# Optimization experiments

Hardware: AMD Instinct MI355X
Metric: run time of the kernel (lower is better)

## Reference

```python
import jax, jax.numpy as jnp
import numpy as np

N_NODES = 50000
N_EDGES = 300000
EMB = 256
HID = 512
L = 5
BN_EPS = 1e-5


def setup_inputs() -> dict:
    key = jax.random.key(0)
    ks = jax.random.split(key, 12)
    return {
        "node_ids": jax.random.randint(ks[0], (N_NODES,), 0, 100),
        "node_depth": jax.random.randint(ks[1], (N_NODES,), 0, 20),
        "edge_index": jax.random.randint(ks[2], (2, N_EDGES), 0, N_NODES),
        "edge_attr": jax.random.normal(ks[3], (N_EDGES, 2), jnp.float32),
        "node_type_emb": jax.random.normal(ks[4], (100, EMB), jnp.float32) * 0.1,
        "depth_emb": jax.random.normal(ks[5], (21, EMB), jnp.float32) * 0.1,
        "We": jax.random.normal(ks[6], (L, 2, EMB), jnp.float32) * 0.1,
        "be": jnp.zeros((L, EMB), jnp.float32),
        "W1": jax.random.normal(ks[7], (L, EMB, HID), jnp.float32) * (1.0 / np.sqrt(EMB)),
        "b1": jnp.zeros((L, HID), jnp.float32),
        "gamma": jnp.ones((L, HID), jnp.float32),
        "beta": jnp.zeros((L, HID), jnp.float32),
        "W2": jax.random.normal(ks[8], (L, HID, EMB), jnp.float32) * (1.0 / np.sqrt(HID)),
        "b2": jnp.zeros((L, EMB), jnp.float32),
        "eps_param": jnp.zeros((L,), jnp.float32),
    }


def reference(node_ids, node_depth, edge_index, edge_attr, node_type_emb,
              depth_emb, We, be, W1, b1, gamma, beta, W2, b2, eps_param):
    n = node_ids.shape[0]
    src, dst = edge_index[0], edge_index[1]
    # node encoder (code task): type embedding + clipped depth embedding
    depth = jnp.clip(node_depth, 0, depth_emb.shape[0] - 1)
    h = node_type_emb[node_ids] + depth_emb[depth]  # [N, EMB]
    n_layers = We.shape[0]
    for l in range(n_layers):
        e = edge_attr @ We[l] + be[l]  # [E, EMB] edge encoding
        msg = jax.nn.relu(h[src] + e)  # gather + relu
        agg = jax.ops.segment_sum(msg, dst, num_segments=n)  # scatter-add
        z = (1.0 + eps_param[l]) * h + agg
        # MLP: Linear -> BatchNorm1d (batch stats) -> ReLU -> Linear
        y = z @ W1[l] + b1[l]  # [N, HID]
        mu = jnp.mean(y, axis=0)
        var = jnp.var(y, axis=0)
        y = (y - mu) * jax.lax.rsqrt(var + BN_EPS) * gamma[l] + beta[l]
        y = jax.nn.relu(y)
        h_new = y @ W2[l] + b2[l]  # [N, EMB]
        if l < n_layers - 1:
            h_new = jax.nn.relu(h_new)  # dropout is identity (drop_ratio=0)
        h = h_new
    return h
```

## Files before the change

kernel.cpp:

```cpp
#include <hip/hip_runtime.h>

#define NN 50000
#define NE 300000
#define EMB 256
#define HID 512
#define NL 5

typedef __attribute__((ext_vector_type(8))) short bf16x8;
typedef __attribute__((ext_vector_type(4))) float f32x4;
typedef __attribute__((ext_vector_type(8))) unsigned short u16x8;
typedef __attribute__((ext_vector_type(4))) unsigned short u16x4;

union U8u { u16x8 v; unsigned short s[8]; };

__device__ __forceinline__ float bf2f(unsigned short u) {
  union { unsigned int i; float f; } c; c.i = ((unsigned int)u) << 16; return c.f;
}
__device__ __forceinline__ unsigned short f2bf(float f) {
  union { float f; unsigned int i; } c; c.f = f;
  unsigned int r = c.i + 0x7FFF + ((c.i >> 16) & 1);
  return (unsigned short)(r >> 16);
}

__global__ __launch_bounds__(256) void k_init_h(const int* __restrict__ ids,
    const int* __restrict__ depth, const float* __restrict__ temb,
    const float* __restrict__ demb, float* __restrict__ h) {
  int gid = blockIdx.x * 256 + threadIdx.x;
  int row = gid >> 6;
  if (row >= NN) return;
  int c4 = (gid & 63) << 2;
  int id = ids[row];
  int d = depth[row]; d = d < 0 ? 0 : (d > 20 ? 20 : d);
  float4 a = *(const float4*)&temb[id * EMB + c4];
  float4 b = *(const float4*)&demb[d * EMB + c4];
  *(float4*)&h[row * EMB + c4] = make_float4(a.x + b.x, a.y + b.y, a.z + b.z, a.w + b.w);
}

__global__ __launch_bounds__(256) void k_count(const int* __restrict__ dst, int* __restrict__ deg) {
  int e = blockIdx.x * 256 + threadIdx.x;
  if (e < NE) atomicAdd(&deg[dst[e]], 1);
}
__global__ __launch_bounds__(256) void k_scan1(const int* __restrict__ deg,
    int* __restrict__ row_off, int* __restrict__ bsums) {
  __shared__ int lds[256];
  int b = blockIdx.x, t = threadIdx.x;
  int base = b * 1024;
  int v[4]; int s = 0;
  for (int i = 0; i < 4; ++i) {
    int idx = base + t * 4 + i;
    v[i] = (idx < NN) ? deg[idx] : 0;
    s += v[i];
  }
  lds[t] = s; __syncthreads();
  for (int off = 1; off < 256; off <<= 1) {
    int x = (t >= off) ? lds[t - off] : 0; __syncthreads();
    lds[t] += x; __syncthreads();
  }
  int run = (t > 0) ? lds[t - 1] : 0;
  if (t == 255) bsums[b] = lds[255];
  for (int i = 0; i < 4; ++i) {
    int idx = base + t * 4 + i;
    if (idx < NN) row_off[idx] = run;
    run += v[i];
  }
}
__global__ __launch_bounds__(256) void k_scan2(int* __restrict__ bsums, int nb) {
  __shared__ int lds[256];
  int t = threadIdx.x;
  int v = (t < nb) ? bsums[t] : 0;
  lds[t] = v; __syncthreads();
  for (int off = 1; off < 256; off <<= 1) {
    int x = (t >= off) ? lds[t - off] : 0; __syncthreads();
    lds[t] += x; __syncthreads();
  }
  if (t < nb) bsums[t] = (t > 0) ? lds[t - 1] : 0;
}
__global__ __launch_bounds__(256) void k_scan3(int* __restrict__ row_off, const int* __restrict__ bsums) {
  int b = blockIdx.x, t = threadIdx.x;
  int base = b * 1024;
  int add = bsums[b];
  for (int i = 0; i < 4; ++i) {
    int idx = base + t * 4 + i;
    if (idx < NN) row_off[idx] += add;
  }
  if (b == 0 && t == 0) row_off[NN] = NE;
}
__global__ __launch_bounds__(256) void k_copy(const int* __restrict__ a, int* __restrict__ b) {
  int i = blockIdx.x * 256 + threadIdx.x;
  if (i < NN) b[i] = a[i];
}
__global__ __launch_bounds__(256) void k_fill(const int* __restrict__ src, const int* __restrict__ dst,
    const float* __restrict__ attr, int* __restrict__ cursor,
    int* __restrict__ ssrc, float2* __restrict__ sattr) {
  int e = blockIdx.x * 256 + threadIdx.x;
  if (e >= NE) return;
  int d = dst[e];
  int p = atomicAdd(&cursor[d], 1);
  ssrc[p] = src[e];
  sattr[p] = make_float2(attr[2 * e], attr[2 * e + 1]);
}

__global__ __launch_bounds__(256) void k_convW(const float* __restrict__ W,
    unsigned short* __restrict__ Wt, int R, int C) {
  __shared__ float t[32][33];
  int l = blockIdx.z;
  const float* Wl = W + (size_t)l * R * C;
  unsigned short* Wtl = Wt + (size_t)l * R * C;
  int c0 = blockIdx.x * 32, r0 = blockIdx.y * 32;
  int tx = threadIdx.x & 31, ty = threadIdx.x >> 5;
  for (int i = 0; i < 32; i += 8)
    t[ty + i][tx] = Wl[(size_t)(r0 + ty + i) * C + c0 + tx];
  __syncthreads();
  for (int i = 0; i < 32; i += 8)
    Wtl[(size_t)(c0 + ty + i) * R + r0 + tx] = f2bf(t[tx][ty + i]);
}

__global__ __launch_bounds__(256) void k_aggregate(const float* __restrict__ h,
    const int* __restrict__ row_off, const int* __restrict__ ssrc,
    const float2* __restrict__ sattr, const float* __restrict__ We_l,
    const float* __restrict__ be_l, const float* __restrict__ epsp, int layer,
    unsigned short* __restrict__ z) {
  int wid = (blockIdx.x * 256 + threadIdx.x) >> 6;
  if (wid >= NN) return;
  int c4 = (threadIdx.x & 63) << 2;
  float4 w0 = *(const float4*)&We_l[c4];
  float4 w1 = *(const float4*)&We_l[EMB + c4];
  float4 bb = *(const float4*)&be_l[c4];
  float4 acc = make_float4(0.f, 0.f, 0.f, 0.f);
  int k0 = row_off[wid], k1 = row_off[wid + 1];
  for (int k = k0; k < k1; ++k) {
    int s = ssrc[k];
    float2 a = sattr[k];
    float4 hv = *(const float4*)&h[(size_t)s * EMB + c4];
    acc.x += fmaxf(hv.x + a.x * w0.x + a.y * w1.x + bb.x, 0.f);
    acc.y += fmaxf(hv.y + a.x * w0.y + a.y * w1.y + bb.y, 0.f);
    acc.z += fmaxf(hv.z + a.x * w0.z + a.y * w1.z + bb.z, 0.f);
    acc.w += fmaxf(hv.w + a.x * w0.w + a.y * w1.w + bb.w, 0.f);
  }
  float e1 = 1.0f + epsp[layer];
  float4 hv = *(const float4*)&h[(size_t)wid * EMB + c4];
  u16x4 o;
  o[0] = f2bf(e1 * hv.x + acc.x);
  o[1] = f2bf(e1 * hv.y + acc.y);
  o[2] = f2bf(e1 * hv.z + acc.z);
  o[3] = f2bf(e1 * hv.w + acc.w);
  *(u16x4*)&z[(size_t)wid * EMB + c4] = o;
}

template<int K, int NC, int MODE>
__global__ __launch_bounds__(256) void k_mfma_gemm(
    const unsigned short* __restrict__ A, const unsigned short* __restrict__ Bt,
    const float* __restrict__ bias, const float* __restrict__ scale,
    const float* __restrict__ shift, unsigned short* __restrict__ Ybf,
    float* __restrict__ Hout, float* __restrict__ colsum, float* __restrict__ colsq) {
  __shared__ __align__(16) unsigned short lA[2][128 * 32];
  __shared__ __align__(16) unsigned short lB[2][128 * 32];
  int row0 = blockIdx.x * 128, col0 = blockIdx.y * 128;
  int tid = threadIdx.x, lane = tid & 63, wave = tid >> 6;
  int wr = (wave >> 1) * 64, wc = (wave & 1) * 64;
  int lr = lane & 15, lg = lane >> 4;
  f32x4 acc[4][4] = {};

  auto stageA = [&](int buf, int k0) {
#pragma unroll
    for (int r = 0; r < 2; ++r) {
      int off8 = (r * 256 + tid) * 8;
      int row = off8 >> 5;
      int kk = off8 & 31;
      int gr = row0 + row; if (gr > NN - 1) gr = NN - 1;
      u16x8 v = *(const u16x8*)&A[(size_t)gr * K + k0 + kk];
      if constexpr (MODE >= 1) {
        f32x4 sc0 = *(const f32x4*)&scale[k0 + kk];
        f32x4 sc1 = *(const f32x4*)&scale[k0 + kk + 4];
        f32x4 sh0 = *(const f32x4*)&shift[k0 + kk];
        f32x4 sh1 = *(const f32x4*)&shift[k0 + kk + 4];
        U8u u; u.v = v;
#pragma unroll
        for (int j = 0; j < 4; ++j)
          u.s[j] = f2bf(fmaxf(bf2f(u.s[j]) * sc0[j] + sh0[j], 0.f));
#pragma unroll
        for (int j = 0; j < 4; ++j)
          u.s[4 + j] = f2bf(fmaxf(bf2f(u.s[4 + j]) * sc1[j] + sh1[j], 0.f));
        v = u.v;
      }
      *(u16x8*)&lA[buf][off8] = v;
    }
  };
  auto stageB = [&](int buf, int k0) {
#pragma unroll
    for (int r = 0; r < 2; ++r) {
      int off8 = (r * 256 + tid) * 8;
      int col = off8 >> 5;
      int kk = off8 & 31;
      *(u16x8*)&lB[buf][off8] = *(const u16x8*)&Bt[(size_t)(col0 + col) * K + k0 + kk];
    }
  };

  int cur = 0;
  stageA(0, 0); stageB(0, 0);
  __syncthreads();
  for (int kt = 0; kt < K / 32; ++kt) {
    if (kt + 1 < K / 32) { stageA(cur ^ 1, (kt + 1) * 32); stageB(cur ^ 1, (kt + 1) * 32); }
    bf16x8 af[4], bfr[4];
#pragma unroll
    for (int m = 0; m < 4; ++m)
      af[m] = *(const bf16x8*)&lA[cur][(wr + m * 16 + lr) * 32 + lg * 8];
#pragma unroll
    for (int n = 0; n < 4; ++n)
      bfr[n] = *(const bf16x8*)&lB[cur][(wc + n * 16 + lr) * 32 + lg * 8];
#pragma unroll
    for (int m = 0; m < 4; ++m)
#pragma unroll
      for (int n = 0; n < 4; ++n)
        acc[m][n] = __builtin_amdgcn_mfma_f32_16x16x32_bf16(af[m], bfr[n], acc[m][n], 0, 0, 0);
    __syncthreads();
    cur ^= 1;
  }

  if constexpr (MODE == 0) {
    float cs[4] = {}, cq[4] = {};
#pragma unroll
    for (int n = 0; n < 4; ++n) {
      int gc = col0 + wc + n * 16 + lr;
      float bv = bias[gc];
#pragma unroll
      for (int m = 0; m < 4; ++m) {
        int grb = row0 + wr + m * 16 + lg * 4;
#pragma unroll
        for (int j = 0; j < 4; ++j) {
          int gr = grb + j;
          if (gr < NN) {
            float v = acc[m][n][j] + bv;
            Ybf[(size_t)gr * NC + gc] = f2bf(v);
            cs[n] += v; cq[n] += v * v;
          }
        }
      }
    }
#pragma unroll
    for (int n = 0; n < 4; ++n) {
      cs[n] += __shfl_xor(cs[n], 16, 64); cs[n] += __shfl_xor(cs[n], 32, 64);
      cq[n] += __shfl_xor(cq[n], 16, 64); cq[n] += __shfl_xor(cq[n], 32, 64);
    }
    if (lg == 0) {
#pragma unroll
      for (int n = 0; n < 4; ++n) {
        int gc = col0 + wc + n * 16 + lr;
        atomicAdd(&colsum[gc], cs[n]);
        atomicAdd(&colsq[gc], cq[n]);
      }
    }
  } else {
#pragma unroll
    for (int n = 0; n < 4; ++n) {
      int gc = col0 + wc + n * 16 + lr;
      float bv = bias[gc];
#pragma unroll
      for (int m = 0; m < 4; ++m) {
        int grb = row0 + wr + m * 16 + lg * 4;
#pragma unroll
        for (int j = 0; j < 4; ++j) {
          int gr = grb + j;
          if (gr < NN) {
            float v = acc[m][n][j] + bv;
            if constexpr (MODE == 1) v = fmaxf(v, 0.f);
            Hout[(size_t)gr * NC + gc] = v;
          }
        }
      }
    }
  }
}

__global__ void k_bnfin(const float* __restrict__ colsum, const float* __restrict__ colsq,
    const float* __restrict__ gamma, const float* __restrict__ beta,
    float* __restrict__ scale, float* __restrict__ shift) {
  int c = threadIdx.x;
  float inv_n = 1.0f / (float)NN;
  float mu = colsum[c] * inv_n;
  float var = colsq[c] * inv_n - mu * mu;
  float rstd = rsqrtf(var + 1e-5f);
  float sc = rstd * gamma[c];
  scale[c] = sc;
  shift[c] = beta[c] - mu * sc;
}

extern "C" void kernel_launch(void* const* d_in, const int* in_sizes, int n_in,
                              void* d_out, int out_size, void* d_ws, size_t ws_size,
                              hipStream_t stream) {
  (void)in_sizes; (void)n_in; (void)out_size; (void)ws_size;
  const int* node_ids    = (const int*)d_in[0];
  const int* node_depth  = (const int*)d_in[1];
  const int* edge_index  = (const int*)d_in[2];
  const float* edge_attr = (const float*)d_in[3];
  const float* temb      = (const float*)d_in[4];
  const float* demb      = (const float*)d_in[5];
  const float* We        = (const float*)d_in[6];
  const float* be        = (const float*)d_in[7];
  const float* W1        = (const float*)d_in[8];
  const float* b1        = (const float*)d_in[9];
  const float* gamma_    = (const float*)d_in[10];
  const float* beta_     = (const float*)d_in[11];
  const float* W2        = (const float*)d_in[12];
  const float* b2        = (const float*)d_in[13];
  const float* epsp      = (const float*)d_in[14];
  float* h = (float*)d_out;

  char* ws = (char*)d_ws;
  size_t off = 0;
  auto alloc = [&](size_t bytes) -> void* {
    void* p = ws + off;
    off = (off + bytes + 255) & ~(size_t)255;
    return p;
  };
  unsigned short* z   = (unsigned short*)alloc(2ull * NN * EMB);
  unsigned short* y   = (unsigned short*)alloc(2ull * NN * HID);
  unsigned short* W1t = (unsigned short*)alloc(2ull * NL * EMB * HID);
  unsigned short* W2t = (unsigned short*)alloc(2ull * NL * HID * EMB);
  int* deg      = (int*)alloc(sizeof(int) * NN);
  int* row_off  = (int*)alloc(sizeof(int) * (NN + 1));
  int* cursor   = (int*)alloc(sizeof(int) * NN);
  int* ssrc     = (int*)alloc(sizeof(int) * NE);
  float2* sattr = (float2*)alloc(sizeof(float2) * NE);
  int* bsums    = (int*)alloc(sizeof(int) * 256);
  float* colsum = (float*)alloc(sizeof(float) * HID * 2);
  float* colsq  = colsum + HID;
  float* scale  = (float*)alloc(sizeof(float) * HID);
  float* shift  = (float*)alloc(sizeof(float) * HID);

  const int* e_src = edge_index;
  const int* e_dst = edge_index + NE;

  k_init_h<<<(NN * 64) / 256, 256, 0, stream>>>(node_ids, node_depth, temb, demb, h);
  hipMemsetAsync(deg, 0, sizeof(int) * NN, stream);
  k_count<<<(NE + 255) / 256, 256, 0, stream>>>(e_dst, deg);
  k_scan1<<<49, 256, 0, stream>>>(deg, row_off, bsums);
  k_scan2<<<1, 256, 0, stream>>>(bsums, 49);
  k_scan3<<<49, 256, 0, stream>>>(row_off, bsums);
  k_copy<<<(NN + 255) / 256, 256, 0, stream>>>(row_off, cursor);
  k_fill<<<(NE + 255) / 256, 256, 0, stream>>>(e_src, e_dst, edge_attr, cursor, ssrc, sattr);
  k_convW<<<dim3(HID / 32, EMB / 32, NL), 256, 0, stream>>>(W1, W1t, EMB, HID);
  k_convW<<<dim3(EMB / 32, HID / 32, NL), 256, 0, stream>>>(W2, W2t, HID, EMB);

  const int MB = (NN + 127) / 128;
  for (int l = 0; l < NL; ++l) {
    k_aggregate<<<(NN * 64) / 256, 256, 0, stream>>>(
        h, row_off, ssrc, sattr, We + (size_t)l * 2 * EMB, be + (size_t)l * EMB, epsp, l, z);
    hipMemsetAsync(colsum, 0, sizeof(float) * HID * 2, stream);
    k_mfma_gemm<EMB, HID, 0><<<dim3(MB, HID / 128), 256, 0, stream>>>(
        z, W1t + (size_t)l * EMB * HID, b1 + (size_t)l * HID,
        nullptr, nullptr, y, nullptr, colsum, colsq);
    k_bnfin<<<1, HID, 0, stream>>>(colsum, colsq, gamma_ + (size_t)l * HID,
                                   beta_ + (size_t)l * HID, scale, shift);
    if (l < NL - 1)
      k_mfma_gemm<HID, EMB, 1><<<dim3(MB, EMB / 128), 256, 0, stream>>>(
          y, W2t + (size_t)l * HID * EMB, b2 + (size_t)l * EMB,
          scale, shift, nullptr, h, nullptr, nullptr);
    else
      k_mfma_gemm<HID, EMB, 2><<<dim3(MB, EMB / 128), 256, 0, stream>>>(
          y, W2t + (size_t)l * HID * EMB, b2 + (size_t)l * EMB,
          scale, shift, nullptr, h, nullptr, nullptr);
  }
}
```

Baseline: 1.132 ms.

## Restructure MFMA GEMMs to keep whole B panel in LDS and stream A from registers

The GEMM kernel is rewritten so each block preloads its entire weight column panel (all K) into shared memory once, with fragments pre-arranged in MFMA lane order. A operands are loaded directly from global into registers with a 3-deep prefetch ring, so the per-k-step LDS staging and barriers go away. Each wave owns 32 rows across the full column tile. The first GEMM's output is staged through LDS for 16-byte vectorized bf16 stores, and the second GEMM uses 64-wide column tiles. The cost is larger LDS use per block, which may lower occupancy, and A rows are re-read from global by every column block.

After: 1.403 ms. 1.24x slower.

```diff
diff --git a/kernel.cpp b/kernel.cpp
--- a/kernel.cpp
+++ b/kernel.cpp
@@ -11,7 +11,7 @@
 typedef __attribute__((ext_vector_type(8))) unsigned short u16x8;
 typedef __attribute__((ext_vector_type(4))) unsigned short u16x4;
 
-union U8u { u16x8 v; unsigned short s[8]; };
+union U8u { u16x8 v; bf16x8 b; unsigned short s[8]; };
 
 __device__ __forceinline__ float bf2f(unsigned short u) {
   union { unsigned int i; float f; } c; c.i = ((unsigned int)u) << 16; return c.f;
@@ -147,117 +147,134 @@
   *(u16x4*)&z[(size_t)wid * EMB + c4] = o;
 }
 
-template<int K, int NC, int MODE>
-__global__ __launch_bounds__(256) void k_mfma_gemm(
+template<int K, int NC, int NF, int MODE>
+__global__ __launch_bounds__(256) void k_gemm(
     const unsigned short* __restrict__ A, const unsigned short* __restrict__ Bt,
     const float* __restrict__ bias, const float* __restrict__ scale,
     const float* __restrict__ shift, unsigned short* __restrict__ Ybf,
     float* __restrict__ Hout, float* __restrict__ colsum, float* __restrict__ colsq) {
-  __shared__ __align__(16) unsigned short lA[2][128 * 32];
-  __shared__ __align__(16) unsigned short lB[2][128 * 32];
-  int row0 = blockIdx.x * 128, col0 = blockIdx.y * 128;
+  constexpr int KT = K / 32;
+  constexpr int CB = NF * 16;
+  __shared__ __align__(16) unsigned short ldsB[KT * NF * 512];
   int tid = threadIdx.x, lane = tid & 63, wave = tid >> 6;
-  int wr = (wave >> 1) * 64, wc = (wave & 1) * 64;
+  int row0 = blockIdx.x * 128, col0 = blockIdx.y * CB;
   int lr = lane & 15, lg = lane >> 4;
-  f32x4 acc[4][4] = {};
-
-  auto stageA = [&](int buf, int k0) {
-#pragma unroll
-    for (int r = 0; r < 2; ++r) {
-      int off8 = (r * 256 + tid) * 8;
-      int row = off8 >> 5;
-      int kk = off8 & 31;
-      int gr = row0 + row; if (gr > NN - 1) gr = NN - 1;
-      u16x8 v = *(const u16x8*)&A[(size_t)gr * K + k0 + kk];
-      if constexpr (MODE >= 1) {
-        f32x4 sc0 = *(const f32x4*)&scale[k0 + kk];
-        f32x4 sc1 = *(const f32x4*)&scale[k0 + kk + 4];
-        f32x4 sh0 = *(const f32x4*)&shift[k0 + kk];
-        f32x4 sh1 = *(const f32x4*)&shift[k0 + kk + 4];
-        U8u u; u.v = v;
-#pragma unroll
-        for (int j = 0; j < 4; ++j)
-          u.s[j] = f2bf(fmaxf(bf2f(u.s[j]) * sc0[j] + sh0[j], 0.f));
-#pragma unroll
-        for (int j = 0; j < 4; ++j)
-          u.s[4 + j] = f2bf(fmaxf(bf2f(u.s[4 + j]) * sc1[j] + sh1[j], 0.f));
-        v = u.v;
+
+  constexpr int NCH = KT * NF * 64;
+#pragma unroll
+  for (int it = 0; it < NCH / 256; ++it) {
+    int i16 = it * 256 + tid;
+    int frag = i16 >> 6, l = i16 & 63;
+    int n = frag % NF, kt = frag / NF;
+    int col = col0 + n * 16 + (l & 15);
+    int k = kt * 32 + (l >> 4) * 8;
+    *(u16x8*)&ldsB[i16 * 8] = *(const u16x8*)&Bt[(size_t)col * K + k];
+  }
+  __syncthreads();
+
+  int row0w = row0 + wave * 32;
+  int r0 = row0w + lr;      if (r0 > NN - 1) r0 = NN - 1;
+  int r1 = row0w + 16 + lr; if (r1 > NN - 1) r1 = NN - 1;
+  const unsigned short* a0p = A + (size_t)r0 * K + lg * 8;
+  const unsigned short* a1p = A + (size_t)r1 * K + lg * 8;
+
+  f32x4 acc[2][NF] = {};
+  u16x8 ap0[3], ap1[3];
+  ap0[0] = *(const u16x8*)(a0p);
+  ap1[0] = *(const u16x8*)(a1p);
+  ap0[1] = *(const u16x8*)(a0p + 32);
+  ap1[1] = *(const u16x8*)(a1p + 32);
+  ap0[2] = *(const u16x8*)(a0p + 64);
+  ap1[2] = *(const u16x8*)(a1p + 64);
+
+#pragma unroll
+  for (int kt = 0; kt < KT; ++kt) {
+    U8u am0, am1;
+    am0.v = ap0[kt % 3]; am1.v = ap1[kt % 3];
+    if (kt + 3 < KT) {
+      ap0[kt % 3] = *(const u16x8*)(a0p + (kt + 3) * 32);
+      ap1[kt % 3] = *(const u16x8*)(a1p + (kt + 3) * 32);
+    }
+    bf16x8 af0, af1;
+    if constexpr (MODE >= 1) {
+      int kb = kt * 32 + lg * 8;
+      f32x4 sc0 = *(const f32x4*)&scale[kb], sc1 = *(const f32x4*)&scale[kb + 4];
+      f32x4 sh0 = *(const f32x4*)&shift[kb], sh1 = *(const f32x4*)&shift[kb + 4];
+      U8u o0, o1;
+#pragma unroll
+      for (int j = 0; j < 4; ++j) {
+        o0.s[j]     = f2bf(fmaxf(bf2f(am0.s[j])     * sc0[j] + sh0[j], 0.f));
+        o0.s[4 + j] = f2bf(fmaxf(bf2f(am0.s[4 + j]) * sc1[j] + sh1[j], 0.f));
+        o1.s[j]     = f2bf(fmaxf(bf2f(am1.s[j])     * sc0[j] + sh0[j], 0.f));
+        o1.s[4 + j] = f2bf(fmaxf(bf2f(am1.s[4 + j]) * sc1[j] + sh1[j], 0.f));
       }
-      *(u16x8*)&lA[buf][off8] = v;
-    }
-  };
-  auto stageB = [&](int buf, int k0) {
-#pragma unroll
-    for (int r = 0; r < 2; ++r) {
-      int off8 = (r * 256 + tid) * 8;
-      int col = off8 >> 5;
-      int kk = off8 & 31;
-      *(u16x8*)&lB[buf][off8] = *(const u16x8*)&Bt[(size_t)(col0 + col) * K + k0 + kk];
-    }
-  };
-
-  int cur = 0;
-  stageA(0, 0); stageB(0, 0);
-  __syncthreads();
-  for (int kt = 0; kt < K / 32; ++kt) {
-    if (kt + 1 < K / 32) { stageA(cur ^ 1, (kt + 1) * 32); stageB(cur ^ 1, (kt + 1) * 32); }
-    bf16x8 af[4], bfr[4];
-#pragma unroll
-    for (int m = 0; m < 4; ++m)
-      af[m] = *(const bf16x8*)&lA[cur][(wr + m * 16 + lr) * 32 + lg * 8];
-#pragma unroll
-    for (int n = 0; n < 4; ++n)
-      bfr[n] = *(const bf16x8*)&lB[cur][(wc + n * 16 + lr) * 32 + lg * 8];
-#pragma unroll
-    for (int m = 0; m < 4; ++m)
-#pragma unroll
-      for (int n = 0; n < 4; ++n)
-        acc[m][n] = __builtin_amdgcn_mfma_f32_16x16x32_bf16(af[m], bfr[n], acc[m][n], 0, 0, 0);
+      af0 = o0.b; af1 = o1.b;
+    } else {
+      af0 = am0.b; af1 = am1.b;
+    }
+    const unsigned short* bb = &ldsB[(kt * NF) * 512 + lane * 8];
+#pragma unroll
+    for (int n = 0; n < NF; ++n) {
+      U8u bu; bu.v = *(const u16x8*)(bb + n * 512);
+      acc[0][n] = __builtin_amdgcn_mfma_f32_16x16x32_bf16(af0, bu.b, acc[0][n], 0, 0, 0);
+      acc[1][n] = __builtin_amdgcn_mfma_f32_16x16x32_bf16(af1, bu.b, acc[1][n], 0, 0, 0);
+    }
+  }
+
+  if constexpr (MODE == 0) {
     __syncthreads();
-    cur ^= 1;
-  }
-
-  if constexpr (MODE == 0) {
-    float cs[4] = {}, cq[4] = {};
-#pragma unroll
-    for (int n = 0; n < 4; ++n) {
-      int gc = col0 + wc + n * 16 + lr;
-      float bv = bias[gc];
-#pragma unroll
-      for (int m = 0; m < 4; ++m) {
-        int grb = row0 + wr + m * 16 + lg * 4;
+    float* ldsW = (float*)&ldsB[0] + wave * (32 * CB);
+    float cs[NF], cq[NF];
+#pragma unroll
+    for (int n = 0; n < NF; ++n) { cs[n] = 0.f; cq[n] = 0.f; }
+#pragma unroll
+    for (int n = 0; n < NF; ++n) {
+      float bv = bias[col0 + n * 16 + lr];
+#pragma unroll
+      for (int m = 0; m < 2; ++m)
 #pragma unroll
         for (int j = 0; j < 4; ++j) {
-          int gr = grb + j;
-          if (gr < NN) {
-            float v = acc[m][n][j] + bv;
-            Ybf[(size_t)gr * NC + gc] = f2bf(v);
-            cs[n] += v; cq[n] += v * v;
-          }
+          float v = acc[m][n][j] + bv;
+          int gr = row0w + m * 16 + lg * 4 + j;
+          if (gr < NN) { cs[n] += v; cq[n] += v * v; }
+          ldsW[(m * 16 + lg * 4 + j) * CB + n * 16 + lr] = v;
         }
-      }
-    }
-#pragma unroll
-    for (int n = 0; n < 4; ++n) {
+    }
+#pragma unroll
+    for (int n = 0; n < NF; ++n) {
       cs[n] += __shfl_xor(cs[n], 16, 64); cs[n] += __shfl_xor(cs[n], 32, 64);
       cq[n] += __shfl_xor(cq[n], 16, 64); cq[n] += __shfl_xor(cq[n], 32, 64);
     }
     if (lg == 0) {
 #pragma unroll
-      for (int n = 0; n < 4; ++n) {
-        int gc = col0 + wc + n * 16 + lr;
-        atomicAdd(&colsum[gc], cs[n]);
-        atomicAdd(&colsq[gc], cq[n]);
+      for (int n = 0; n < NF; ++n) {
+        atomicAdd(&colsum[col0 + n * 16 + lr], cs[n]);
+        atomicAdd(&colsq[col0 + n * 16 + lr], cq[n]);
       }
     }
+    asm volatile("s_waitcnt lgkmcnt(0)" ::: "memory");
+#pragma unroll
+    for (int it = 0; it < (32 * CB) / 512; ++it) {
+      int e = it * 512 + lane * 8;
+      int row = e / CB, colr = e % CB;
+      int gr = row0w + row;
+      if (gr < NN) {
+        f32x4 v0 = *(const f32x4*)&ldsW[e];
+        f32x4 v1 = *(const f32x4*)&ldsW[e + 4];
+        U8u o;
+#pragma unroll
+        for (int j = 0; j < 4; ++j) { o.s[j] = f2bf(v0[j]); o.s[4 + j] = f2bf(v1[j]); }
+        *(u16x8*)&Ybf[(size_t)gr * NC + col0 + colr] = o.v;
+      }
+    }
   } else {
 #pragma unroll
-    for (int n = 0; n < 4; ++n) {
-      int gc = col0 + wc + n * 16 + lr;
+    for (int n = 0; n < NF; ++n) {
+      int gc = col0 + n * 16 + lr;
       float bv = bias[gc];
 #pragma unroll
-      for (int m = 0; m < 4; ++m) {
-        int grb = row0 + wr + m * 16 + lg * 4;
+      for (int m = 0; m < 2; ++m) {
+        int grb = row0w + m * 16 + lg * 4;
 #pragma unroll
         for (int j = 0; j < 4; ++j) {
           int gr = grb + j;
@@ -347,17 +364,17 @@
     k_aggregate<<<(NN * 64) / 256, 256, 0, stream>>>(
         h, row_off, ssrc, sattr, We + (size_t)l * 2 * EMB, be + (size_t)l * EMB, epsp, l, z);
     hipMemsetAsync(colsum, 0, sizeof(float) * HID * 2, stream);
-    k_mfma_gemm<EMB, HID, 0><<<dim3(MB, HID / 128), 256, 0, stream>>>(
+    k_gemm<EMB, HID, 8, 0><<<dim3(MB, HID / 128), 256, 0, stream>>>(
         z, W1t + (size_t)l * EMB * HID, b1 + (size_t)l * HID,
         nullptr, nullptr, y, nullptr, colsum, colsq);
     k_bnfin<<<1, HID, 0, stream>>>(colsum, colsq, gamma_ + (size_t)l * HID,
                                    beta_ + (size_t)l * HID, scale, shift);
     if (l < NL - 1)
-      k_mfma_gemm<HID, EMB, 1><<<dim3(MB, EMB / 128), 256, 0, stream>>>(
+      k_gemm<HID, EMB, 4, 1><<<dim3(MB, EMB / 64), 256, 0, stream>>>(
           y, W2t + (size_t)l * HID * EMB, b2 + (size_t)l * EMB,
           scale, shift, nullptr, h, nullptr, nullptr);
     else
-      k_mfma_gemm<HID, EMB, 2><<<dim3(MB, EMB / 128), 256, 0, stream>>>(
+      k_gemm<HID, EMB, 4, 2><<<dim3(MB, EMB / 64), 256, 0, stream>>>(
           y, W2t + (size_t)l * HID * EMB, b2 + (size_t)l * EMB,
           scale, shift, nullptr, h, nullptr, nullptr);
   }
```

## Register-prefetch GEMM tiles, swap MFMA operands for vector stores, reorder grid

Applied to the files above, without the earlier changes.

The GEMM now loads the next K-tile from global memory into registers before the MFMA loop and writes it to LDS afterwards, so global-load latency overlaps with compute instead of stalling before it. Swapping the MFMA operands transposes the accumulator layout, so each lane holds four consecutive columns; the epilogue can then use vector bias loads and vector bf16/f32 stores, with the column-stat reduction moved to shuffles across lanes. The grid is also reordered so column tiles vary fastest, letting blocks that share A rows run close together for better L2 reuse. The cost is higher register pressure from the prefetch buffers and the scale/shift vectors.

After: 1.250 ms. 1.1x slower.

```diff
diff --git a/kernel.cpp b/kernel.cpp
--- a/kernel.cpp
+++ b/kernel.cpp
@@ -11,7 +11,7 @@
 typedef __attribute__((ext_vector_type(8))) unsigned short u16x8;
 typedef __attribute__((ext_vector_type(4))) unsigned short u16x4;
 
-union U8u { u16x8 v; unsigned short s[8]; };
+union U8u { u16x8 v; bf16x8 b; unsigned short s[8]; };
 
 __device__ __forceinline__ float bf2f(unsigned short u) {
   union { unsigned int i; float f; } c; c.i = ((unsigned int)u) << 16; return c.f;
@@ -148,124 +148,137 @@
 }
 
 template<int K, int NC, int MODE>
-__global__ __launch_bounds__(256) void k_mfma_gemm(
+__global__ __launch_bounds__(256) void k_gemm(
     const unsigned short* __restrict__ A, const unsigned short* __restrict__ Bt,
     const float* __restrict__ bias, const float* __restrict__ scale,
     const float* __restrict__ shift, unsigned short* __restrict__ Ybf,
     float* __restrict__ Hout, float* __restrict__ colsum, float* __restrict__ colsq) {
+  constexpr int KT = K / 32;
   __shared__ __align__(16) unsigned short lA[2][128 * 32];
   __shared__ __align__(16) unsigned short lB[2][128 * 32];
-  int row0 = blockIdx.x * 128, col0 = blockIdx.y * 128;
-  int tid = threadIdx.x, lane = tid & 63, wave = tid >> 6;
-  int wr = (wave >> 1) * 64, wc = (wave & 1) * 64;
-  int lr = lane & 15, lg = lane >> 4;
+  const int tid = threadIdx.x;
+  const int lane = tid & 63, wave = tid >> 6;
+  const int lr = lane & 15, lg = lane >> 4;
+  const int wr = (wave >> 1) * 64, wc = (wave & 1) * 64;
+  const int col0 = blockIdx.x * 128, row0 = blockIdx.y * 128;
+
+  const int rA = tid >> 1;
+  const int hA = (tid & 1) * 16;
+  int grs = row0 + rA; if (grs > NN - 1) grs = NN - 1;
+  const unsigned short* aSrc = A + (size_t)grs * K + hA;
+  const unsigned short* bSrc = Bt + (size_t)(col0 + rA) * K + hA;
+  unsigned short* aDst = &lA[0][0] + rA * 32 + hA;
+  unsigned short* bDst = &lB[0][0] + rA * 32 + hA;
+
   f32x4 acc[4][4] = {};
-
-  auto stageA = [&](int buf, int k0) {
-#pragma unroll
-    for (int r = 0; r < 2; ++r) {
-      int off8 = (r * 256 + tid) * 8;
-      int row = off8 >> 5;
-      int kk = off8 & 31;
-      int gr = row0 + row; if (gr > NN - 1) gr = NN - 1;
-      u16x8 v = *(const u16x8*)&A[(size_t)gr * K + k0 + kk];
-      if constexpr (MODE >= 1) {
-        f32x4 sc0 = *(const f32x4*)&scale[k0 + kk];
-        f32x4 sc1 = *(const f32x4*)&scale[k0 + kk + 4];
-        f32x4 sh0 = *(const f32x4*)&shift[k0 + kk];
-        f32x4 sh1 = *(const f32x4*)&shift[k0 + kk + 4];
-        U8u u; u.v = v;
-#pragma unroll
-        for (int j = 0; j < 4; ++j)
-          u.s[j] = f2bf(fmaxf(bf2f(u.s[j]) * sc0[j] + sh0[j], 0.f));
-#pragma unroll
-        for (int j = 0; j < 4; ++j)
-          u.s[4 + j] = f2bf(fmaxf(bf2f(u.s[4 + j]) * sc1[j] + sh1[j], 0.f));
-        v = u.v;
-      }
-      *(u16x8*)&lA[buf][off8] = v;
+  u16x8 ra0, ra1, rb0, rb1;
+  f32x4 sc[4], sh[4];
+
+  auto tload = [&](int kt) {
+    ra0 = *(const u16x8*)(aSrc + kt * 32);
+    ra1 = *(const u16x8*)(aSrc + kt * 32 + 8);
+    rb0 = *(const u16x8*)(bSrc + kt * 32);
+    rb1 = *(const u16x8*)(bSrc + kt * 32 + 8);
+    if constexpr (MODE >= 1) {
+      int kb = kt * 32 + hA;
+#pragma unroll
+      for (int q = 0; q < 4; ++q) {
+        sc[q] = *(const f32x4*)&scale[kb + q * 4];
+        sh[q] = *(const f32x4*)&shift[kb + q * 4];
+      }
     }
   };
-  auto stageB = [&](int buf, int k0) {
-#pragma unroll
-    for (int r = 0; r < 2; ++r) {
-      int off8 = (r * 256 + tid) * 8;
-      int col = off8 >> 5;
-      int kk = off8 & 31;
-      *(u16x8*)&lB[buf][off8] = *(const u16x8*)&Bt[(size_t)(col0 + col) * K + k0 + kk];
+  auto twrite = [&](int buf) {
+    u16x8 wa0 = ra0, wa1 = ra1;
+    if constexpr (MODE >= 1) {
+      U8u a0, a1, o0, o1;
+      a0.v = ra0; a1.v = ra1;
+#pragma unroll
+      for (int j = 0; j < 4; ++j) {
+        o0.s[j]     = f2bf(fmaxf(bf2f(a0.s[j])     * sc[0][j] + sh[0][j], 0.f));
+        o0.s[4 + j] = f2bf(fmaxf(bf2f(a0.s[4 + j]) * sc[1][j] + sh[1][j], 0.f));
+        o1.s[j]     = f2bf(fmaxf(bf2f(a1.s[j])     * sc[2][j] + sh[2][j], 0.f));
+        o1.s[4 + j] = f2bf(fmaxf(bf2f(a1.s[4 + j]) * sc[3][j] + sh[3][j], 0.f));
+      }
+      wa0 = o0.v; wa1 = o1.v;
     }
+    *(u16x8*)(aDst + buf * 4096) = wa0;
+    *(u16x8*)(aDst + buf * 4096 + 8) = wa1;
+    *(u16x8*)(bDst + buf * 4096) = rb0;
+    *(u16x8*)(bDst + buf * 4096 + 8) = rb1;
   };
 
-  int cur = 0;
-  stageA(0, 0); stageB(0, 0);
+  tload(0); twrite(0);
   __syncthreads();
-  for (int kt = 0; kt < K / 32; ++kt) {
-    if (kt + 1 < K / 32) { stageA(cur ^ 1, (kt + 1) * 32); stageB(cur ^ 1, (kt + 1) * 32); }
+  int buf = 0;
+  for (int kt = 0; kt < KT; ++kt) {
+    if (kt + 1 < KT) tload(kt + 1);
     bf16x8 af[4], bfr[4];
 #pragma unroll
     for (int m = 0; m < 4; ++m)
-      af[m] = *(const bf16x8*)&lA[cur][(wr + m * 16 + lr) * 32 + lg * 8];
+      af[m] = *(const bf16x8*)&lA[buf][(wr + m * 16 + lr) * 32 + lg * 8];
 #pragma unroll
     for (int n = 0; n < 4; ++n)
-      bfr[n] = *(const bf16x8*)&lB[cur][(wc + n * 16 + lr) * 32 + lg * 8];
+      bfr[n] = *(const bf16x8*)&lB[buf][(wc + n * 16 + lr) * 32 + lg * 8];
 #pragma unroll
     for (int m = 0; m < 4; ++m)
 #pragma unroll
       for (int n = 0; n < 4; ++n)
-        acc[m][n] = __builtin_amdgcn_mfma_f32_16x16x32_bf16(af[m], bfr[n], acc[m][n], 0, 0, 0);
+        acc[m][n] = __builtin_amdgcn_mfma_f32_16x16x32_bf16(bfr[n], af[m], acc[m][n], 0, 0, 0);
+    if (kt + 1 < KT) twrite(buf ^ 1);
     __syncthreads();
-    cur ^= 1;
+    buf ^= 1;
   }
 
   if constexpr (MODE == 0) {
-    float cs[4] = {}, cq[4] = {};
+    f32x4 csum[4] = {}, csq[4] = {};
 #pragma unroll
     for (int n = 0; n < 4; ++n) {
-      int gc = col0 + wc + n * 16 + lr;
-      float bv = bias[gc];
+      const int gcB = col0 + wc + n * 16 + lg * 4;
+      f32x4 bv = *(const f32x4*)&bias[gcB];
 #pragma unroll
       for (int m = 0; m < 4; ++m) {
-        int grb = row0 + wr + m * 16 + lg * 4;
-#pragma unroll
-        for (int j = 0; j < 4; ++j) {
-          int gr = grb + j;
-          if (gr < NN) {
-            float v = acc[m][n][j] + bv;
-            Ybf[(size_t)gr * NC + gc] = f2bf(v);
-            cs[n] += v; cq[n] += v * v;
+        int gr = row0 + wr + m * 16 + lr;
+        if (gr < NN) {
+          f32x4 v = acc[m][n] + bv;
+          u16x4 o;
+#pragma unroll
+          for (int j = 0; j < 4; ++j) o[j] = f2bf(v[j]);
+          *(u16x4*)&Ybf[(size_t)gr * NC + gcB] = o;
+          csum[n] += v;
+          csq[n] += v * v;
+        }
+      }
+    }
+#pragma unroll
+    for (int n = 0; n < 4; ++n)
+#pragma unroll
+      for (int j = 0; j < 4; ++j) {
+        float s = csum[n][j], q = csq[n][j];
+        s += __shfl_xor(s, 1, 64); q += __shfl_xor(q, 1, 64);
+        s += __shfl_xor(s, 2, 64); q += __shfl_xor(q, 2, 64);
+        s += __shfl_xor(s, 4, 64); q += __shfl_xor(q, 4, 64);
+        s += __shfl_xor(s, 8, 64); q += __shfl_xor(q, 8, 64);
+        if (lr == 0) {
+          atomicAdd(&colsum[col0 + wc + n * 16 + lg * 4 + j], s);
+          atomicAdd(&colsq[col0 + wc + n * 16 + lg * 4 + j], q);
+        }
+      }
+  } else {
+#pragma unroll
+    for (int n = 0; n < 4; ++n) {
+      const int gcB = col0 + wc + n * 16 + lg * 4;
+      f32x4 bv = *(const f32x4*)&bias[gcB];
+#pragma unroll
+      for (int m = 0; m < 4; ++m) {
+        int gr = row0 + wr + m * 16 + lr;
+        if (gr < NN) {
+          f32x4 v = acc[m][n] + bv;
+          if constexpr (MODE == 1) {
+#pragma unroll
+            for (int j = 0; j < 4; ++j) v[j] = fmaxf(v[j], 0.f);
           }
-        }
-      }
-    }
-#pragma unroll
-    for (int n = 0; n < 4; ++n) {
-      cs[n] += __shfl_xor(cs[n], 16, 64); cs[n] += __shfl_xor(cs[n], 32, 64);
-      cq[n] += __shfl_xor(cq[n], 16, 64); cq[n] += __shfl_xor(cq[n], 32, 64);
-    }
-    if (lg == 0) {
-#pragma unroll
-      for (int n = 0; n < 4; ++n) {
-        int gc = col0 + wc + n * 16 + lr;
-        atomicAdd(&colsum[gc], cs[n]);
-        atomicAdd(&colsq[gc], cq[n]);
-      }
-    }
-  } else {
-#pragma unroll
-    for (int n = 0; n < 4; ++n) {
-      int gc = col0 + wc + n * 16 + lr;
-      float bv = bias[gc];
-#pragma unroll
-      for (int m = 0; m < 4; ++m) {
-        int grb = row0 + wr + m * 16 + lg * 4;
-#pragma unroll
-        for (int j = 0; j < 4; ++j) {
-          int gr = grb + j;
-          if (gr < NN) {
-            float v = acc[m][n][j] + bv;
-            if constexpr (MODE == 1) v = fmaxf(v, 0.f);
-            Hout[(size_t)gr * NC + gc] = v;
-          }
+          *(f32x4*)&Hout[(size_t)gr * NC + gcB] = v;
         }
       }
     }
@@ -347,17 +360,17 @@
     k_aggregate<<<(NN * 64) / 256, 256, 0, stream>>>(
         h, row_off, ssrc, sattr, We + (size_t)l * 2 * EMB, be + (size_t)l * EMB, epsp, l, z);
     hipMemsetAsync(colsum, 0, sizeof(float) * HID * 2, stream);
-    k_mfma_gemm<EMB, HID, 0><<<dim3(MB, HID / 128), 256, 0, stream>>>(
+    k_gemm<EMB, HID, 0><<<dim3(HID / 128, MB), 256, 0, stream>>>(
         z, W1t + (size_t)l * EMB * HID, b1 + (size_t)l * HID,
         nullptr, nullptr, y, nullptr, colsum, colsq);
     k_bnfin<<<1, HID, 0, stream>>>(colsum, colsq, gamma_ + (size_t)l * HID,
                                    beta_ + (size_t)l * HID, scale, shift);
     if (l < NL - 1)
-      k_mfma_gemm<HID, EMB, 1><<<dim3(MB, EMB / 128), 256, 0, stream>>>(
+      k_gemm<HID, EMB, 1><<<dim3(EMB / 128, MB), 256, 0, stream>>>(
           y, W2t + (size_t)l * HID * EMB, b2 + (size_t)l * EMB,
           scale, shift, nullptr, h, nullptr, nullptr);
     else
-      k_mfma_gemm<HID, EMB, 2><<<dim3(MB, EMB / 128), 256, 0, stream>>>(
+      k_gemm<HID, EMB, 2><<<dim3(EMB / 128, MB), 256, 0, stream>>>(
           y, W2t + (size_t)l * HID * EMB, b2 + (size_t)l * EMB,
           scale, shift, nullptr, h, nullptr, nullptr);
   }
```
